# Kernel tuning notes

Measured on AMD Instinct MI355X. Metric: run time of the kernel, lower is better.

The kernel has to match this reference:

```python
import jax, jax.numpy as jnp
import numpy as np

B, S, HID = 1, 4096, 2048
NH, NKV, HD = 16, 4, 128
BLK, LOCAL, GNB, STRIDE = 64, 4, 2, 4
ROT = 64  # head_dim * rope_partial_rotary_factor(0.5), already even
SCALE = HD ** -0.5
NEG = -1e9


def _block_select(nb):
    """Static local+global key-block selection per query block (mirrors _select_key_blocks)."""
    sels = []
    for bi in range(nb):
        local = list(range(max(0, bi - LOCAL + 1), bi + 1))
        gc = list(range(0, bi + 1, STRIDE))
        if len(gc) > GNB:
            gc = gc[-GNB:]
        if 0 not in gc:
            gc = [0] + gc
        idx = sorted(set(local + gc))
        sels.append([i for i in idx if 0 <= i < nb and i <= bi])
    m = max(len(s) for s in sels)
    idx = np.zeros((nb, m), np.int32)
    valid = np.zeros((nb, m), bool)
    for i, s in enumerate(sels):
        idx[i, :len(s)] = s
        valid[i, :len(s)] = True
    return jnp.asarray(idx), jnp.asarray(valid)


def _rot_half(x):
    h = x.shape[-1] // 2
    return jnp.concatenate([-x[..., h:], x[..., :h]], axis=-1)


def setup_inputs() -> dict:
    key = jax.random.key(0)
    ks = jax.random.split(key, 8)
    w = lambda k, shp: (jax.random.normal(k, shp, jnp.float32) * 0.02)
    return {
        "hidden": jax.random.normal(ks[0], (B, S, HID), jnp.float32),
        "cos": jax.random.uniform(ks[1], (B, S, ROT), jnp.float32, -1.0, 1.0),
        "sin": jax.random.uniform(ks[2], (B, S, ROT), jnp.float32, -1.0, 1.0),
        "Wq": w(ks[3], (HID, NH * HD)),
        "Wk": w(ks[4], (HID, NKV * HD)),
        "Wv": w(ks[5], (HID, NKV * HD)),
        "Wo": w(ks[6], (NH * HD, HID)),
        "attn_mask": jnp.ones((B, S), jnp.float32),
    }


def reference(hidden, cos, sin, Wq, Wk, Wv, Wo, attn_mask):
    b_, s_, _ = hidden.shape
    q = (hidden @ Wq).reshape(b_, s_, NH, HD).transpose(0, 2, 1, 3)   # [B,H,S,d]
    k = (hidden @ Wk).reshape(b_, s_, NKV, HD).transpose(0, 2, 1, 3)  # [B,Hkv,S,d]
    v = (hidden @ Wv).reshape(b_, s_, NKV, HD).transpose(0, 2, 1, 3)

    # partial RoPE on first ROT channels
    c = cos[:, None, :, :]
    sn = sin[:, None, :, :]
    q1, q2 = q[..., :ROT], q[..., ROT:]
    k1, k2 = k[..., :ROT], k[..., ROT:]
    q = jnp.concatenate([q1 * c + _rot_half(q1) * sn, q2], axis=-1)
    k = jnp.concatenate([k1 * c + _rot_half(k1) * sn, k2], axis=-1)

    # repeat_kv (GQA expand: each kv head repeated contiguously)
    rep = NH // NKV
    k = jnp.repeat(k, rep, axis=1)
    v = jnp.repeat(v, rep, axis=1)

    nb = s_ // BLK  # S chosen divisible by BLK (pad_len == 0)
    qb = q.reshape(b_, NH, nb, BLK, HD)
    kb = k.reshape(b_, NH, nb, BLK, HD)
    vb = v.reshape(b_, NH, nb, BLK, HD)

    idx, valid = _block_select(nb)  # [nb, M]
    m = idx.shape[1]
    ksel = kb[:, :, idx]  # [B,H,nb,M,BLK,d]
    vsel = vb[:, :, idx]

    scores = jnp.einsum('bhnqd,bhnmkd->bhnqmk',
                        qb.astype(jnp.float32), ksel.astype(jnp.float32)) * SCALE
    # key-validity (padding) mask, additive as in original
    key_valid = attn_mask.reshape(b_, nb, BLK)
    kvm = key_valid[:, idx]  # [B,nb,M,BLK]
    scores = scores + (1.0 - kvm[:, None, :, None, :, :]) * NEG
    # invalid (padded) selected slots
    scores = jnp.where(valid[None, None, :, None, :, None], scores, NEG)
    # intra-block causal mask on the diagonal block
    intra = jnp.triu(jnp.ones((BLK, BLK), bool), 1)                    # [q,k]
    same = idx == jnp.arange(nb)[:, None]                              # [nb,M]
    diag = same[:, None, :, None] & intra[None, :, None, :]            # [nb,q,M,k]
    scores = jnp.where(diag[None, None], NEG, scores)

    probs = jax.nn.softmax(scores.reshape(b_, NH, nb, BLK, m * BLK), axis=-1)
    vflat = vsel.reshape(b_, NH, nb, m * BLK, HD)
    out = jnp.einsum('bhnqe,bhned->bhnqd', probs.astype(v.dtype), vflat)
    out = out.reshape(b_, NH, s_, HD).transpose(0, 2, 1, 3).reshape(b_, s_, NH * HD)
    return out @ Wo
```

## Files before the change

### kernel.cpp

```cpp
#include <hip/hip_runtime.h>
#include <hip/hip_bf16.h>


typedef short short8 __attribute__((ext_vector_type(8)));
typedef float f32x4  __attribute__((ext_vector_type(4)));

#define NEGV   (-1.0e9f)
#define SCALE  (0.08838834764831845f)

__device__ __forceinline__ void gload16(const void* g, void* l) {
  __builtin_amdgcn_global_load_lds(
      (const __attribute__((address_space(1))) unsigned int*)g,
      (__attribute__((address_space(3))) unsigned int*)l, 16, 0, 0);
}

__device__ __forceinline__ float bf2f(short s) {
  union { unsigned u; float f; } c;
  c.u = ((unsigned)(unsigned short)s) << 16;
  return c.f;
}

__device__ __forceinline__ short f2bf_s(float f) {
  __hip_bfloat16 b = __float2bfloat16(f);
  short s;
  __builtin_memcpy(&s, &b, 2);
  return s;
}

__global__ void prep_all(const float* __restrict__ H, const float* __restrict__ Wq,
                         const float* __restrict__ Wk, const float* __restrict__ Wv,
                         const float* __restrict__ Wo, __hip_bfloat16* __restrict__ X,
                         __hip_bfloat16* __restrict__ Wt, __hip_bfloat16* __restrict__ Wot) {
  __shared__ __hip_bfloat16 tile[64][73];
  int b = blockIdx.x;
  if (b < 8192) {
    size_t t = (size_t)b * 256 + threadIdx.x;
    float4 v = *(const float4*)(H + t * 4);
    __hip_bfloat16* o = X + t * 4;
    o[0] = __float2bfloat16(v.x); o[1] = __float2bfloat16(v.y);
    o[2] = __float2bfloat16(v.z); o[3] = __float2bfloat16(v.w);
    return;
  }
  const float* src; __hip_bfloat16* dst; int C; int idx;
  if (b < 9216)      { src = Wq; dst = Wt;                          C = 2048; idx = b - 8192; }
  else if (b < 9472) { src = Wk; dst = Wt + (size_t)2048 * 2048;    C = 512;  idx = b - 9216; }
  else if (b < 9728) { src = Wv; dst = Wt + (size_t)2560 * 2048;    C = 512;  idx = b - 9472; }
  else               { src = Wo; dst = Wot;                         C = 2048; idx = b - 9728; }
  int r0 = (idx & 31) * 64, c0 = (idx >> 5) * 64;
  int c = threadIdx.x & 63, rq = threadIdx.x >> 6;
#pragma unroll
  for (int i = 0; i < 16; ++i) {
    int r = i * 4 + rq;
    tile[r][c] = __float2bfloat16(src[(size_t)(r0 + r) * C + c0 + c]);
  }
  __syncthreads();
#pragma unroll
  for (int i = 0; i < 16; ++i) {
    int cc = i * 4 + rq;
    dst[(size_t)(c0 + cc) * 2048 + r0 + c] = tile[c][cc];
  }
}

__global__ void postproc(const float* __restrict__ cosb, const float* __restrict__ sinb,
                         __hip_bfloat16* __restrict__ Qb, __hip_bfloat16* __restrict__ Kb,
                         const __hip_bfloat16* __restrict__ Vb, __hip_bfloat16* __restrict__ Vt) {
  __shared__ __hip_bfloat16 tile[64][73];
  int blk = blockIdx.x;
  if (blk < 1280) {
    int t = blk * 256 + threadIdx.x;
    __hip_bfloat16* p;
    int s;
    if (t < 262144) {
      s = t >> 6;
      int rem = t & 63;
      p = Qb + (size_t)s * 2048 + (rem >> 2) * 128 + (rem & 3) * 8;
    } else {
      int tk = t - 262144;
      s = tk >> 4;
      int rem = tk & 15;
      p = Kb + (size_t)s * 512 + (rem >> 2) * 128 + (rem & 3) * 8;
    }
    const int g8 = (t & 3) * 8;
    const float* cp = cosb + (size_t)s * 64 + g8;
    const float* sp = sinb + (size_t)s * 64 + g8;
    short8 a = *(const short8*)p;
    short8 b = *(const short8*)(p + 32);
    float ca[8], sa[8], cb[8], sb[8];
    *(float4*)&ca[0] = *(const float4*)cp;        *(float4*)&ca[4] = *(const float4*)(cp + 4);
    *(float4*)&cb[0] = *(const float4*)(cp + 32); *(float4*)&cb[4] = *(const float4*)(cp + 36);
    *(float4*)&sa[0] = *(const float4*)sp;        *(float4*)&sa[4] = *(const float4*)(sp + 4);
    *(float4*)&sb[0] = *(const float4*)(sp + 32); *(float4*)&sb[4] = *(const float4*)(sp + 36);
    short8 oa, ob;
#pragma unroll
    for (int i = 0; i < 8; ++i) {
      float av = bf2f(a[i]), bv = bf2f(b[i]);
      oa[i] = f2bf_s(av * ca[i] - bv * sa[i]);
      ob[i] = f2bf_s(bv * cb[i] + av * sb[i]);
    }
    *(short8*)p = oa;
    *(short8*)(p + 32) = ob;
    return;
  }
  int idx = blk - 1280;
  int s0 = (idx & 63) * 64, c0 = (idx >> 6) * 64;
  int c = threadIdx.x & 63, rq = threadIdx.x >> 6;
#pragma unroll
  for (int i = 0; i < 16; ++i) {
    int r = i * 4 + rq;
    tile[r][c] = Vb[(size_t)(s0 + r) * 512 + c0 + c];
  }
  __syncthreads();
#pragma unroll
  for (int i = 0; i < 16; ++i) {
    int cc = i * 4 + rq;
    Vt[(size_t)(c0 + cc) * 4096 + s0 + c] = tile[c][cc];
  }
}

__global__ __launch_bounds__(512, 2) void gemm_qkv4p(
    const __hip_bfloat16* __restrict__ A, const __hip_bfloat16* __restrict__ Bt,
    __hip_bfloat16* __restrict__ Qb, __hip_bfloat16* __restrict__ Kb,
    __hip_bfloat16* __restrict__ Vb) {
  const int K = 2048;
  const int tid = threadIdx.x;
  const int wave = tid >> 6, lane = tid & 63;
  const int l15 = lane & 15, lg = lane >> 4;
  const int bm = blockIdx.x, bn = blockIdx.y;
  const int wm = wave >> 2, wn = wave & 3;

  __shared__ __hip_bfloat16 lds[65536];

  f32x4 acc[8][4] = {};
  const int srow = lane >> 3;
  const int sslot = lane & 7;
  const int scol = (sslot ^ srow) * 8;
  const size_t abase = (size_t)bm * 256 * K;
  const size_t bbase = (size_t)bn * 256 * K;
  const int r3 = l15 & 7;

#define STAGE_HALF(SRC, SBASE, HALF, KO, LBASE)                                  \
  {                                                                              \
    _Pragma("unroll")                                                            \
    for (int l = 0; l < 2; ++l) {                                                \
      int chunk = l * 8 + wave;                                                  \
      int row = chunk * 8 + srow;                                                \
      gload16(SRC + (SBASE) + (size_t)((HALF) * 128 + row) * K + (KO) + scol,    \
              &lds[(LBASE) + chunk * 512]);                                      \
    }                                                                            \
  }

  short8 bfr[4][2];
  short8 af[2][2][2];

#define READ_AF(P, Q, BA)                                                        \
  {                                                                              \
    _Pragma("unroll")                                                            \
    for (int m2 = 0; m2 < 2; ++m2)                                               \
      _Pragma("unroll")                                                          \
      for (int ks = 0; ks < 2; ++ks) {                                           \
        int row = ((Q) * 2 + m2) * 16 + l15;                                     \
        int slot = (ks * 4 + lg) ^ r3;                                           \
        af[P][m2][ks] = *(const short8*)&lds[(BA) + row * 64 + slot * 8];        \
      }                                                                          \
  }

#define READ_BF(BB)                                                              \
  {                                                                              \
    _Pragma("unroll")                                                            \
    for (int ni = 0; ni < 4; ++ni)                                               \
      _Pragma("unroll")                                                          \
      for (int ks = 0; ks < 2; ++ks) {                                           \
        int row = (wn & 1) * 64 + ni * 16 + l15;                                 \
        int slot = (ks * 4 + lg) ^ r3;                                           \
        bfr[ni][ks] = *(const short8*)&lds[(BB) + row * 64 + slot * 8];          \
      }                                                                          \
  }

#define MFMA_Q(Q, P)                                                             \
  {                                                                              \
    __builtin_amdgcn_s_setprio(1);                                               \
    _Pragma("unroll")                                                            \
    for (int ks = 0; ks < 2; ++ks)                                               \
      _Pragma("unroll")                                                          \
      for (int m2 = 0; m2 < 2; ++m2)                                             \
        _Pragma("unroll")                                                        \
        for (int ni = 0; ni < 4; ++ni)                                           \
          acc[(Q) * 2 + m2][ni] = __builtin_amdgcn_mfma_f32_16x16x32_bf16(       \
              af[P][m2][ks], bfr[ni][ks], acc[(Q) * 2 + m2][ni], 0, 0, 0);       \
    __builtin_amdgcn_s_setprio(0);                                               \
  }

#define LGKM0()                                                                  \
  asm volatile("s_waitcnt lgkmcnt(0)" ::: "memory");                             \
  __builtin_amdgcn_sched_barrier(0);

  STAGE_HALF(Bt, bbase, 0, 0, 16384);
  STAGE_HALF(Bt, bbase, 1, 0, 24576);
  STAGE_HALF(A, abase, 0, 0, 0);
  STAGE_HALF(A, abase, 1, 0, 8192);
  STAGE_HALF(Bt, bbase, 0, 64, 49152);
  STAGE_HALF(Bt, bbase, 1, 64, 57344);
  asm volatile("s_waitcnt vmcnt(4)" ::: "memory");
  __builtin_amdgcn_sched_barrier(0);
  __builtin_amdgcn_s_barrier();
  {
    const int bA0 = wm * 8192;
    const int bB0 = 16384 + (wn >> 1) * 8192;
    READ_BF(bB0);
    READ_AF(0, 0, bA0);
  }
  LGKM0();

  for (int t = 0; t < 32; ++t) {
    const int buf = (t & 1) * 32768;
    const int nbuf = buf ^ 32768;
    const int bA = buf + wm * 8192;
    if (t + 1 < 32) STAGE_HALF(A, abase, 0, (t + 1) * 64, nbuf);
    __builtin_amdgcn_s_barrier();
    MFMA_Q(0, 0);
    READ_AF(1, 1, bA);
    LGKM0();
    if (t + 1 < 32) STAGE_HALF(A, abase, 1, (t + 1) * 64, nbuf + 8192);
    __builtin_amdgcn_s_barrier();
    MFMA_Q(1, 1);
    READ_AF(0, 2, bA);
    LGKM0();
    if (t + 2 < 32) STAGE_HALF(Bt, bbase, 0, (t + 2) * 64, buf + 16384);
    __builtin_amdgcn_s_barrier();
    MFMA_Q(2, 0);
    READ_AF(1, 3, bA);
    LGKM0();
    if (t + 2 < 32) STAGE_HALF(Bt, bbase, 1, (t + 2) * 64, buf + 24576);
    if (t < 30) asm volatile("s_waitcnt vmcnt(4)" ::: "memory");
    else        asm volatile("s_waitcnt vmcnt(0)" ::: "memory");
    __builtin_amdgcn_sched_barrier(0);
    __builtin_amdgcn_s_barrier();
    MFMA_Q(3, 1);
    if (t + 1 < 32) {
      const int nbA = nbuf + wm * 8192;
      const int nbB = nbuf + 16384 + (wn >> 1) * 8192;
      READ_BF(nbB);
      READ_AF(0, 0, nbA);
    }
    LGKM0();
  }
#undef STAGE_HALF
#undef READ_AF
#undef READ_BF
#undef MFMA_Q
#undef LGKM0

  __hip_bfloat16* dst; int ldc, coff;
  if (bn < 8)       { dst = Qb; ldc = 2048; coff = bn * 256; }
  else if (bn < 10) { dst = Kb; ldc = 512;  coff = bn * 256 - 2048; }
  else              { dst = Vb; ldc = 512;  coff = bn * 256 - 2560; }
#pragma unroll
  for (int m8 = 0; m8 < 8; ++m8)
#pragma unroll
    for (int ni = 0; ni < 4; ++ni) {
      int row = bm * 256 + wm * 128 + m8 * 16 + lg * 4;
      int col = coff + wn * 64 + ni * 16 + l15;
#pragma unroll
      for (int r = 0; r < 4; ++r)
        dst[(size_t)(row + r) * ldc + col] = __float2bfloat16(acc[m8][ni][r]);
    }
}

__global__ __launch_bounds__(256) void gemm_bt(
    const __hip_bfloat16* __restrict__ A, const __hip_bfloat16* __restrict__ Bt,
    float* __restrict__ C, int M, int N, int K) {
  const int tid = threadIdx.x;
  const int wave = tid >> 6, lane = tid & 63;
  const int l15 = lane & 15, lg = lane >> 4;
  const int bm = blockIdx.x, bn = blockIdx.y;
  const int wm = wave >> 1, wn = wave & 1;

  __shared__ __hip_bfloat16 As[128 * 64];
  __shared__ __hip_bfloat16 Bs[128 * 64];

  f32x4 acc[4][4] = {};
  const int lrow = lane >> 3;
  const int lslot = lane & 7;
  const int scol = (lslot ^ lrow) * 8;
  const size_t abase = (size_t)bm * 128 * K;
  const size_t bbase = (size_t)bn * 128 * K;
  const int r3 = l15 & 7;

  for (int k0 = 0; k0 < K; k0 += 64) {
#pragma unroll
    for (int i = 0; i < 4; ++i) {
      int seg = i * 4 + wave;
      int row = seg * 8 + lrow;
      gload16(A + abase + (size_t)row * K + k0 + scol, &As[seg * 512]);
      gload16(Bt + bbase + (size_t)row * K + k0 + scol, &Bs[seg * 512]);
    }
    __syncthreads();
#pragma unroll
    for (int ks = 0; ks < 2; ++ks) {
      const int slot = (ks * 4 + lg) ^ r3;
      short8 af[4], bf[4];
#pragma unroll
      for (int mi = 0; mi < 4; ++mi)
        af[mi] = *(const short8*)&As[(wm * 64 + mi * 16 + l15) * 64 + slot * 8];
#pragma unroll
      for (int ni = 0; ni < 4; ++ni)
        bf[ni] = *(const short8*)&Bs[(wn * 64 + ni * 16 + l15) * 64 + slot * 8];
#pragma unroll
      for (int mi = 0; mi < 4; ++mi)
#pragma unroll
        for (int ni = 0; ni < 4; ++ni)
          acc[mi][ni] = __builtin_amdgcn_mfma_f32_16x16x32_bf16(af[mi], bf[ni], acc[mi][ni], 0, 0, 0);
    }
    __syncthreads();
  }
#pragma unroll
  for (int mi = 0; mi < 4; ++mi)
#pragma unroll
    for (int ni = 0; ni < 4; ++ni) {
      int row = bm * 128 + wm * 64 + mi * 16 + lg * 4;
      int col = bn * 128 + wn * 64 + ni * 16 + l15;
#pragma unroll
      for (int r = 0; r < 4; ++r)
        C[(size_t)(row + r) * N + col] = acc[mi][ni][r];
    }
}

__global__ __launch_bounds__(512, 2) void attn_kernel(
    const __hip_bfloat16* __restrict__ Qb,
    const __hip_bfloat16* __restrict__ Kb,
    const __hip_bfloat16* __restrict__ Vt,
    const float* __restrict__ amask,
    __hip_bfloat16* __restrict__ AO)
{
  const int bid = blockIdx.x;
  const int kvh = bid & 3;
  const int bi  = bid >> 2;
  const int tid = threadIdx.x;
  const int wave = tid >> 6, lane = tid & 63;
  const int l15 = lane & 15, lg = lane >> 4;
  const int h  = kvh * 4 + (wave >> 1);
  const int rh = wave & 1;
  const int q0 = bi * 64 + rh * 32;

  int sel[6]; int nsel = 0;
  {
    int gtop = bi >> 2;
    for (int j = 0; j <= bi; ++j) {
      bool pick = (j == 0) || (j >= bi - 3) || (((j & 3) == 0) && ((j >> 2) >= gtop - 1));
      if (pick && nsel < 6) sel[nsel++] = j;
    }
  }

  __shared__ __hip_bfloat16 kv[2][16384];
  __shared__ __hip_bfloat16 Pl[8][2304];

  short8 qf[2][4];
#pragma unroll
  for (int mi = 0; mi < 2; ++mi)
#pragma unroll
    for (int ks = 0; ks < 4; ++ks)
      qf[mi][ks] = *(const short8*)(Qb + (size_t)(q0 + mi * 16 + l15) * 2048 +
                                    h * 128 + ks * 32 + lg * 8);

  float m[2][4], l[2][4];
  f32x4 oacc[2][8] = {};
#pragma unroll
  for (int mi = 0; mi < 2; ++mi)
#pragma unroll
    for (int r = 0; r < 4; ++r) { m[mi][r] = -3.0e38f; l[mi][r] = 0.f; }

#define STAGE_KV(KB, BUF)                                                          \
  {                                                                                \
    _Pragma("unroll")                                                              \
    for (int i = 0; i < 2; ++i) {                                                  \
      int chunk = (i * 8 + wave) * 64 + lane;                                      \
      int row = chunk >> 4, slot = chunk & 15;                                     \
      gload16(Kb + (size_t)((KB) * 64 + row) * 512 + kvh * 128 +                   \
                  ((slot ^ (row & 15)) * 8),                                       \
              &kv[BUF][(i * 8 + wave) * 512]);                                     \
    }                                                                              \
    _Pragma("unroll")                                                              \
    for (int i = 0; i < 2; ++i) {                                                  \
      int chunk = (i * 8 + wave) * 64 + lane;                                      \
      int row = chunk >> 3, slot = chunk & 7;                                      \
      gload16(Vt + (size_t)(kvh * 128 + row) * 4096 + (KB) * 64 +                  \
                  ((slot ^ (row & 7)) * 8),                                        \
              &kv[BUF][8192 + (i * 8 + wave) * 512]);                              \
    }                                                                              \
  }

  STAGE_KV(sel[0], 0);

#pragma unroll
  for (int j = 0; j < 6; ++j) {
    if (j < nsel) {
      const int kb = sel[j];
      if (j + 1 < nsel) {
        STAGE_KV(sel[j + 1], (j + 1) & 1);
        asm volatile("s_waitcnt vmcnt(4)" ::: "memory");
      } else {
        asm volatile("s_waitcnt vmcnt(0)" ::: "memory");
      }
      __builtin_amdgcn_sched_barrier(0);
      __builtin_amdgcn_s_barrier();
      const __hip_bfloat16* kbuf = kv[j & 1];

      f32x4 sc[2][4] = {};
#pragma unroll
      for (int nf = 0; nf < 4; ++nf)
#pragma unroll
        for (int ks = 0; ks < 4; ++ks) {
          short8 b = *(const short8*)&kbuf[(nf * 16 + l15) * 128 +
                                           (((ks * 4 + lg) ^ l15) * 8)];
          sc[0][nf] = __builtin_amdgcn_mfma_f32_16x16x32_bf16(qf[0][ks], b, sc[0][nf], 0, 0, 0);
          sc[1][nf] = __builtin_amdgcn_mfma_f32_16x16x32_bf16(qf[1][ks], b, sc[1][nf], 0, 0, 0);
        }

      float am[4];
#pragma unroll
      for (int nf = 0; nf < 4; ++nf)
        am[nf] = (1.0f - amask[kb * 64 + nf * 16 + l15]) * NEGV;
#pragma unroll
      for (int mi = 0; mi < 2; ++mi)
#pragma unroll
        for (int nf = 0; nf < 4; ++nf) {
          int keyl = nf * 16 + l15;
#pragma unroll
          for (int r = 0; r < 4; ++r) {
            float s = sc[mi][nf][r] * SCALE + am[nf];
            if (kb == bi) {
              int qrow = rh * 32 + mi * 16 + lg * 4 + r;
              if (keyl > qrow) s = NEGV;
            }
            sc[mi][nf][r] = s;
          }
        }

      float pm[2][4];
#pragma unroll
      for (int mi = 0; mi < 2; ++mi)
#pragma unroll
        for (int r = 0; r < 4; ++r) {
          float v = fmaxf(fmaxf(sc[mi][0][r], sc[mi][1][r]),
                          fmaxf(sc[mi][2][r], sc[mi][3][r]));
          v = fmaxf(v, __shfl_xor(v, 1)); v = fmaxf(v, __shfl_xor(v, 2));
          v = fmaxf(v, __shfl_xor(v, 4)); v = fmaxf(v, __shfl_xor(v, 8));
          pm[mi][r] = v;
        }

      bool need = false;
#pragma unroll
      for (int mi = 0; mi < 2; ++mi)
#pragma unroll
        for (int r = 0; r < 4; ++r) need |= (pm[mi][r] - m[mi][r] > 8.0f);
      if (__any(need)) {
#pragma unroll
        for (int mi = 0; mi < 2; ++mi)
#pragma unroll
          for (int r = 0; r < 4; ++r) {
            float mn = fmaxf(m[mi][r], pm[mi][r]);
            float scl = __expf(m[mi][r] - mn);
            l[mi][r] *= scl;
#pragma unroll
            for (int df = 0; df < 8; ++df) oacc[mi][df][r] *= scl;
            m[mi][r] = mn;
          }
      }

#pragma unroll
      for (int mi = 0; mi < 2; ++mi)
#pragma unroll
        for (int r = 0; r < 4; ++r) {
          float rs = 0.f;
#pragma unroll
          for (int nf = 0; nf < 4; ++nf) {
            float p = __expf(sc[mi][nf][r] - m[mi][r]);
            rs += p;
            Pl[wave][(mi * 16 + lg * 4 + r) * 72 + nf * 16 + l15] = __float2bfloat16(p);
          }
          rs += __shfl_xor(rs, 1); rs += __shfl_xor(rs, 2);
          rs += __shfl_xor(rs, 4); rs += __shfl_xor(rs, 8);
          l[mi][r] += rs;
        }

      short8 af2[2][2];
#pragma unroll
      for (int mi = 0; mi < 2; ++mi)
#pragma unroll
        for (int ks = 0; ks < 2; ++ks)
          af2[mi][ks] = *(const short8*)&Pl[wave][(mi * 16 + l15) * 72 + ks * 32 + lg * 8];
#pragma unroll
      for (int df = 0; df < 8; ++df)
#pragma unroll
        for (int ks = 0; ks < 2; ++ks) {
          short8 vb = *(const short8*)&kbuf[8192 + (df * 16 + l15) * 64 +
                                            (((ks * 4 + lg) ^ (l15 & 7)) * 8)];
          oacc[0][df] = __builtin_amdgcn_mfma_f32_16x16x32_bf16(af2[0][ks], vb, oacc[0][df], 0, 0, 0);
          oacc[1][df] = __builtin_amdgcn_mfma_f32_16x16x32_bf16(af2[1][ks], vb, oacc[1][df], 0, 0, 0);
        }
      __builtin_amdgcn_s_barrier();
    }
  }
#undef STAGE_KV

#pragma unroll
  for (int mi = 0; mi < 2; ++mi) {
    float inv[4];
#pragma unroll
    for (int r = 0; r < 4; ++r) inv[r] = 1.0f / l[mi][r];
#pragma unroll
    for (int df = 0; df < 8; ++df)
#pragma unroll
      for (int r = 0; r < 4; ++r) {
        int qrow = q0 + mi * 16 + lg * 4 + r;
        AO[(size_t)qrow * 2048 + h * 128 + df * 16 + l15] =
            __float2bfloat16(oacc[mi][df][r] * inv[r]);
      }
  }
}

extern "C" void kernel_launch(void* const* d_in, const int* in_sizes, int n_in,
                              void* d_out, int out_size, void* d_ws, size_t ws_size,
                              hipStream_t stream) {
  const float* hidden = (const float*)d_in[0];
  const float* cosb   = (const float*)d_in[1];
  const float* sinb   = (const float*)d_in[2];
  const float* Wq     = (const float*)d_in[3];
  const float* Wk     = (const float*)d_in[4];
  const float* Wv     = (const float*)d_in[5];
  const float* Wo     = (const float*)d_in[6];
  const float* amask  = (const float*)d_in[7];

  char* ws = (char*)d_ws;
  __hip_bfloat16* Xb   = (__hip_bfloat16*)(ws);
  __hip_bfloat16* Wt   = (__hip_bfloat16*)(ws + 16777216);
  __hip_bfloat16* Wot  = (__hip_bfloat16*)(ws + 29360128);
  __hip_bfloat16* Qb   = (__hip_bfloat16*)(ws + 37748736);
  __hip_bfloat16* Kb   = (__hip_bfloat16*)(ws + 54525952);
  __hip_bfloat16* Vb   = (__hip_bfloat16*)(ws + 58720256);
  __hip_bfloat16* Vt   = (__hip_bfloat16*)(ws + 62914560);
  __hip_bfloat16* AO   = Xb;

  prep_all<<<10752, 256, 0, stream>>>(hidden, Wq, Wk, Wv, Wo, Xb, Wt, Wot);

  gemm_qkv4p<<<dim3(16, 12), 512, 0, stream>>>(Xb, Wt, Qb, Kb, Vb);

  postproc<<<1792, 256, 0, stream>>>(cosb, sinb, Qb, Kb, Vb, Vt);

  attn_kernel<<<256, 512, 0, stream>>>(Qb, Kb, Vt, amask, AO);

  gemm_bt<<<dim3(32, 16), 256, 0, stream>>>(AO, Wot, (float*)d_out, 4096, 2048, 2048);
}
```

Baseline: 165.5 us.

## Replace 256x256 QKV GEMM with simpler 256x128 double-buffered tiles and swizzled grid

Result: slower. 175.1 us (+5.8%).

```diff
diff --git a/kernel.cpp b/kernel.cpp
--- a/kernel.cpp
+++ b/kernel.cpp
@@ -117,7 +117,7 @@
   }
 }
 
-__global__ __launch_bounds__(512, 2) void gemm_qkv4p(
+__global__ __launch_bounds__(512) void gemm_qkv(
     const __hip_bfloat16* __restrict__ A, const __hip_bfloat16* __restrict__ Bt,
     __hip_bfloat16* __restrict__ Qb, __hip_bfloat16* __restrict__ Kb,
     __hip_bfloat16* __restrict__ Vb) {
@@ -125,144 +125,82 @@
   const int tid = threadIdx.x;
   const int wave = tid >> 6, lane = tid & 63;
   const int l15 = lane & 15, lg = lane >> 4;
-  const int bm = blockIdx.x, bn = blockIdx.y;
-  const int wm = wave >> 2, wn = wave & 3;
-
-  __shared__ __hip_bfloat16 lds[65536];
-
-  f32x4 acc[8][4] = {};
-  const int srow = lane >> 3;
-  const int sslot = lane & 7;
-  const int scol = (sslot ^ srow) * 8;
+  const int j = (blockIdx.x & 7) * 48 + (blockIdx.x >> 3);
+  const int bm = j & 15, bn = j >> 4;
+  const int wm = wave >> 1, wn = wave & 1;
+
+  __shared__ __hip_bfloat16 lds[49152];
+
+  f32x4 acc[4][4] = {};
+  const int lrow = lane >> 3;
+  const int lslot = lane & 7;
+  const int scol = (lslot ^ lrow) * 8;
   const size_t abase = (size_t)bm * 256 * K;
-  const size_t bbase = (size_t)bn * 256 * K;
+  const size_t bbase = (size_t)bn * 128 * K;
   const int r3 = l15 & 7;
 
-#define STAGE_HALF(SRC, SBASE, HALF, KO, LBASE)                                  \
-  {                                                                              \
-    _Pragma("unroll")                                                            \
-    for (int l = 0; l < 2; ++l) {                                                \
-      int chunk = l * 8 + wave;                                                  \
-      int row = chunk * 8 + srow;                                                \
-      gload16(SRC + (SBASE) + (size_t)((HALF) * 128 + row) * K + (KO) + scol,    \
-              &lds[(LBASE) + chunk * 512]);                                      \
-    }                                                                            \
-  }
-
-  short8 bfr[4][2];
-  short8 af[2][2][2];
-
-#define READ_AF(P, Q, BA)                                                        \
-  {                                                                              \
-    _Pragma("unroll")                                                            \
-    for (int m2 = 0; m2 < 2; ++m2)                                               \
-      _Pragma("unroll")                                                          \
-      for (int ks = 0; ks < 2; ++ks) {                                           \
-        int row = ((Q) * 2 + m2) * 16 + l15;                                     \
-        int slot = (ks * 4 + lg) ^ r3;                                           \
-        af[P][m2][ks] = *(const short8*)&lds[(BA) + row * 64 + slot * 8];        \
-      }                                                                          \
-  }
-
-#define READ_BF(BB)                                                              \
-  {                                                                              \
-    _Pragma("unroll")                                                            \
-    for (int ni = 0; ni < 4; ++ni)                                               \
-      _Pragma("unroll")                                                          \
-      for (int ks = 0; ks < 2; ++ks) {                                           \
-        int row = (wn & 1) * 64 + ni * 16 + l15;                                 \
-        int slot = (ks * 4 + lg) ^ r3;                                           \
-        bfr[ni][ks] = *(const short8*)&lds[(BB) + row * 64 + slot * 8];          \
-      }                                                                          \
-  }
-
-#define MFMA_Q(Q, P)                                                             \
-  {                                                                              \
-    __builtin_amdgcn_s_setprio(1);                                               \
-    _Pragma("unroll")                                                            \
-    for (int ks = 0; ks < 2; ++ks)                                               \
-      _Pragma("unroll")                                                          \
-      for (int m2 = 0; m2 < 2; ++m2)                                             \
-        _Pragma("unroll")                                                        \
-        for (int ni = 0; ni < 4; ++ni)                                           \
-          acc[(Q) * 2 + m2][ni] = __builtin_amdgcn_mfma_f32_16x16x32_bf16(       \
-              af[P][m2][ks], bfr[ni][ks], acc[(Q) * 2 + m2][ni], 0, 0, 0);       \
-    __builtin_amdgcn_s_setprio(0);                                               \
-  }
-
-#define LGKM0()                                                                  \
-  asm volatile("s_waitcnt lgkmcnt(0)" ::: "memory");                             \
-  __builtin_amdgcn_sched_barrier(0);
-
-  STAGE_HALF(Bt, bbase, 0, 0, 16384);
-  STAGE_HALF(Bt, bbase, 1, 0, 24576);
-  STAGE_HALF(A, abase, 0, 0, 0);
-  STAGE_HALF(A, abase, 1, 0, 8192);
-  STAGE_HALF(Bt, bbase, 0, 64, 49152);
-  STAGE_HALF(Bt, bbase, 1, 64, 57344);
-  asm volatile("s_waitcnt vmcnt(4)" ::: "memory");
-  __builtin_amdgcn_sched_barrier(0);
-  __builtin_amdgcn_s_barrier();
-  {
-    const int bA0 = wm * 8192;
-    const int bB0 = 16384 + (wn >> 1) * 8192;
-    READ_BF(bB0);
-    READ_AF(0, 0, bA0);
-  }
-  LGKM0();
+#define STAGE_TILE(BUF, KO)                                                        \
+  {                                                                                \
+    _Pragma("unroll")                                                              \
+    for (int i = 0; i < 4; ++i) {                                                  \
+      int seg = i * 8 + wave;                              \
+      int row = seg * 8 + lrow;                                        \
+      gload16(A + abase + (size_t)row * K + (KO) + scol, &lds[(BUF) + seg * 512]); \
+    }                                                                              \
+    _Pragma("unroll")                                                              \
+    for (int i = 0; i < 2; ++i) {                                                  \
+      int seg = i * 8 + wave;                              \
+      int row = seg * 8 + lrow;                                        \
+      gload16(Bt + bbase + (size_t)row * K + (KO) + scol,                          \
+              &lds[(BUF) + 16384 + seg * 512]);                                    \
+    }                                                                              \
+  }
+
+  STAGE_TILE(0, 0);
 
   for (int t = 0; t < 32; ++t) {
-    const int buf = (t & 1) * 32768;
-    const int nbuf = buf ^ 32768;
-    const int bA = buf + wm * 8192;
-    if (t + 1 < 32) STAGE_HALF(A, abase, 0, (t + 1) * 64, nbuf);
+    asm volatile("s_waitcnt vmcnt(0)" ::: "memory");
     __builtin_amdgcn_s_barrier();
-    MFMA_Q(0, 0);
-    READ_AF(1, 1, bA);
-    LGKM0();
-    if (t + 1 < 32) STAGE_HALF(A, abase, 1, (t + 1) * 64, nbuf + 8192);
-    __builtin_amdgcn_s_barrier();
-    MFMA_Q(1, 1);
-    READ_AF(0, 2, bA);
-    LGKM0();
-    if (t + 2 < 32) STAGE_HALF(Bt, bbase, 0, (t + 2) * 64, buf + 16384);
-    __builtin_amdgcn_s_barrier();
-    MFMA_Q(2, 0);
-    READ_AF(1, 3, bA);
-    LGKM0();
-    if (t + 2 < 32) STAGE_HALF(Bt, bbase, 1, (t + 2) * 64, buf + 24576);
-    if (t < 30) asm volatile("s_waitcnt vmcnt(4)" ::: "memory");
-    else        asm volatile("s_waitcnt vmcnt(0)" ::: "memory");
     __builtin_amdgcn_sched_barrier(0);
-    __builtin_amdgcn_s_barrier();
-    MFMA_Q(3, 1);
-    if (t + 1 < 32) {
-      const int nbA = nbuf + wm * 8192;
-      const int nbB = nbuf + 16384 + (wn >> 1) * 8192;
-      READ_BF(nbB);
-      READ_AF(0, 0, nbA);
-    }
-    LGKM0();
-  }
-#undef STAGE_HALF
-#undef READ_AF
-#undef READ_BF
-#undef MFMA_Q
-#undef LGKM0
+    const int buf = (t & 1) ? 24576 : 0;
+    const int nbuf = buf ^ 24576;
+    if (t + 1 < 32) STAGE_TILE(nbuf, (t + 1) * 64);
+    const __hip_bfloat16* As_ = lds + buf;
+    const __hip_bfloat16* Bs_ = lds + buf + 16384;
+#pragma unroll
+    for (int ks = 0; ks < 2; ++ks) {
+      const int slot = (ks * 4 + lg) ^ r3;
+      short8 af[4], bf[4];
+#pragma unroll
+      for (int mi = 0; mi < 4; ++mi)
+        af[mi] = *(const short8*)&As_[(wm * 64 + mi * 16 + l15) * 64 + slot * 8];
+#pragma unroll
+      for (int ni = 0; ni < 4; ++ni)
+        bf[ni] = *(const short8*)&Bs_[(wn * 64 + ni * 16 + l15) * 64 + slot * 8];
+      __builtin_amdgcn_s_setprio(1);
+#pragma unroll
+      for (int mi = 0; mi < 4; ++mi)
+#pragma unroll
+        for (int ni = 0; ni < 4; ++ni)
+          acc[mi][ni] = __builtin_amdgcn_mfma_f32_16x16x32_bf16(af[mi], bf[ni], acc[mi][ni], 0, 0, 0);
+      __builtin_amdgcn_s_setprio(0);
+    }
+  }
+#undef STAGE_TILE
 
   __hip_bfloat16* dst; int ldc, coff;
-  if (bn < 8)       { dst = Qb; ldc = 2048; coff = bn * 256; }
-  else if (bn < 10) { dst = Kb; ldc = 512;  coff = bn * 256 - 2048; }
-  else              { dst = Vb; ldc = 512;  coff = bn * 256 - 2560; }
-#pragma unroll
-  for (int m8 = 0; m8 < 8; ++m8)
+  if (bn < 16)      { dst = Qb; ldc = 2048; coff = bn * 128; }
+  else if (bn < 20) { dst = Kb; ldc = 512;  coff = (bn - 16) * 128; }
+  else              { dst = Vb; ldc = 512;  coff = (bn - 20) * 128; }
+#pragma unroll
+  for (int mi = 0; mi < 4; ++mi)
 #pragma unroll
     for (int ni = 0; ni < 4; ++ni) {
-      int row = bm * 256 + wm * 128 + m8 * 16 + lg * 4;
+      int row = bm * 256 + wm * 64 + mi * 16 + lg * 4;
       int col = coff + wn * 64 + ni * 16 + l15;
 #pragma unroll
       for (int r = 0; r < 4; ++r)
-        dst[(size_t)(row + r) * ldc + col] = __float2bfloat16(acc[m8][ni][r]);
+        dst[(size_t)(row + r) * ldc + col] = __float2bfloat16(acc[mi][ni][r]);
     }
 }
 
@@ -543,7 +481,7 @@
 
   prep_all<<<10752, 256, 0, stream>>>(hidden, Wq, Wk, Wv, Wo, Xb, Wt, Wot);
 
-  gemm_qkv4p<<<dim3(16, 12), 512, 0, stream>>>(Xb, Wt, Qb, Kb, Vb);
+  gemm_qkv<<<384, 512, 0, stream>>>(Xb, Wt, Qb, Kb, Vb);
 
   postproc<<<1792, 256, 0, stream>>>(cosb, sinb, Qb, Kb, Vb, Vt);
 
```
